# Performance work log

Hardware: AMD Instinct MI355X
Metric: run time of the kernel (lower is better)

## Reference

```python
import jax, jax.numpy as jnp
import numpy as np

B, S, D_MODEL, D_K = 16, 2048, 64, 16
HEAD = D_MODEL * D_K  # 1024, width of each of q, k, v


def setup_inputs() -> dict:
    key = jax.random.key(0)
    kx, kw = jax.random.split(key)
    x = jax.random.normal(kx, (B, S, D_MODEL), dtype=jnp.float32)
    # flax Dense kernel: (in_features, features), no bias
    W = jax.random.normal(kw, (D_MODEL, 3 * HEAD), dtype=jnp.float32) / np.sqrt(D_MODEL)
    return {"x": x, "W": W}


def reference(x, W):
    # fused QKV projection (Dense, no bias)
    qkv = jnp.einsum("bsd,df->bsf", x, W)  # [B, S, 3*HEAD]
    q, k, v = jnp.split(qkv, 3, axis=-1)   # each [B, S, HEAD]

    # q @ k^T over the feature dim -> [B, S, S]
    attn = jnp.einsum("bqd,bkd->bqk", q, k)
    # NOTE: original code scales by sqrt(k.shape[0]) == batch size (kept faithfully)
    d_k = k.shape[0]
    attn = attn / jnp.sqrt(jnp.float32(d_k))
    # original masking: keep upper triangle, then send exact zeros to -9e15
    attn = jnp.triu(attn, k=0)
    attn = jnp.where(attn == 0, jnp.float32(-9000000000000000.0), attn)
    attn = jax.nn.softmax(attn, axis=-1)
    return jnp.einsum("bqk,bkd->bqd", attn, v)  # [B, S, HEAD]
```

## Files before the change

kernel.cpp:

```cpp
#include <hip/hip_runtime.h>
#include <math.h>

#define B_ 16
#define S_ 2048
#define DM_ 64
#define HD_ 1024

typedef float floatx4 __attribute__((ext_vector_type(4)));
typedef short bf16x8 __attribute__((ext_vector_type(8)));
typedef unsigned short ushort4v __attribute__((ext_vector_type(4)));
typedef unsigned short ushort8v __attribute__((ext_vector_type(8)));


__device__ __forceinline__ unsigned short bf_hi(float f) {
    return (unsigned short)((__float_as_uint(f) + 0x8000u) >> 16);
}
__device__ __forceinline__ float bf_f(unsigned short h) {
    return __uint_as_float((unsigned)h << 16);
}
__device__ __forceinline__ void cvt4(floatx4 v, ushort4v& h, ushort4v& l) {
    h[0] = bf_hi(v.x); l[0] = bf_hi(v.x - bf_f(h[0]));
    h[1] = bf_hi(v.y); l[1] = bf_hi(v.y - bf_f(h[1]));
    h[2] = bf_hi(v.z); l[2] = bf_hi(v.z - bf_f(h[2]));
    h[3] = bf_hi(v.w); l[3] = bf_hi(v.w - bf_f(h[3]));
}

#define MFMA(a, b, c) __builtin_amdgcn_mfma_f32_16x16x32_bf16((a), (b), (c), 0, 0, 0)

__device__ __forceinline__ int fragidx(int k, int col) {
    return (((col >> 4) * 2 + (k >> 5)) * 64 + ((k >> 3) & 3) * 16 + (col & 15)) * 8
           + (k & 7);
}

__global__ void k_prep(const float* __restrict__ W, unsigned short* __restrict__ ws) {
    unsigned short* Mfh = ws;
    unsigned short* Mfl = ws + 4096;
    unsigned short* Wfh = ws + 8192;
    unsigned short* Wfl = ws + 73728;
    const int bid = blockIdx.x, t = threadIdx.x;
    if (bid < 64) {
        const int d = bid;
        const int e = t;
        const floatx4* wq = (const floatx4*)(W + (size_t)d * 3072);
        const floatx4* wk = (const floatx4*)(W + (size_t)e * 3072 + 1024);
        floatx4 a = {0.f, 0.f, 0.f, 0.f};
#pragma unroll 4
        for (int j = 0; j < 256; ++j) {
            floatx4 qv = wq[j], kv = wk[j];
            a.x = fmaf(qv.x, kv.x, a.x);
            a.y = fmaf(qv.y, kv.y, a.y);
            a.z = fmaf(qv.z, kv.z, a.z);
            a.w = fmaf(qv.w, kv.w, a.w);
        }
        const float v = (a.x + a.y) + (a.z + a.w);
        const int idx = fragidx(d, e);
        const unsigned short hv = bf_hi(v);
        Mfh[idx] = hv;
        Mfl[idx] = bf_hi(v - bf_f(hv));
    } else {
        const int col = (bid - 64) * 64 + t;
#pragma unroll 8
        for (int k = 0; k < 64; ++k) {
            const float v = W[(size_t)k * 3072 + 2048 + col];
            const int idx = fragidx(k, col);
            const unsigned short hv = bf_hi(v);
            Wfh[idx] = hv;
            Wfl[idx] = bf_hi(v - bf_f(hv));
        }
    }
}

__device__ __forceinline__ void stage_tile(
        unsigned short* xrh, unsigned short* xrl,
        unsigned short* xth, unsigned short* xtl,
        int kg, int dc, floatx4 v0, floatx4 v1, floatx4 v2, floatx4 v3) {
    ushort4v h0, l0, h1, l1, h2, l2, h3, l3;
    cvt4(v0, h0, l0); cvt4(v1, h1, l1);
    cvt4(v2, h2, l2); cvt4(v3, h3, l3);
    *(ushort4v*)(xrh + (4 * kg + 0) * 72 + 4 * dc) = h0;
    *(ushort4v*)(xrh + (4 * kg + 1) * 72 + 4 * dc) = h1;
    *(ushort4v*)(xrh + (4 * kg + 2) * 72 + 4 * dc) = h2;
    *(ushort4v*)(xrh + (4 * kg + 3) * 72 + 4 * dc) = h3;
    *(ushort4v*)(xrl + (4 * kg + 0) * 72 + 4 * dc) = l0;
    *(ushort4v*)(xrl + (4 * kg + 1) * 72 + 4 * dc) = l1;
    *(ushort4v*)(xrl + (4 * kg + 2) * 72 + 4 * dc) = l2;
    *(ushort4v*)(xrl + (4 * kg + 3) * 72 + 4 * dc) = l3;
#pragma unroll
    for (int e = 0; e < 4; ++e) {
        ushort4v th = {h0[e], h1[e], h2[e], h3[e]};
        ushort4v tl = {l0[e], l1[e], l2[e], l3[e]};
        const int rT  = 4 * dc + e;
        const int off = rT * 72 + (((kg >> 1) ^ ((rT >> 3) & 3)) << 3)
                      + ((kg & 1) << 2);
        *(ushort4v*)(xth + off) = th;
        *(ushort4v*)(xtl + off) = tl;
    }
}

__global__ __launch_bounds__(512, 1) void k_fused(
        const float* __restrict__ xg, const unsigned short* __restrict__ wsf,
        float* __restrict__ out) {
    __shared__ __align__(16) unsigned short sm[55296];

    const int tid  = threadIdx.x;
    const int h    = tid >> 8;
    const int lt   = tid & 255;
    const int w    = lt >> 6;
    const int wid  = tid >> 6;
    const int lane = tid & 63;
    const int lm   = lane & 15;
    const int lg   = lane >> 4;

    const int bid = blockIdx.x;
    const int qt  = bid >> 4;
    const int bb  = bid & 15;
    const int q0  = qt * 64;
    const int T   = 32 - qt;
    const int nA  = (T + 1) >> 1;
    const int nOwn = h ? (T - nA) : nA;
    const int kt0  = q0 + (h ? nA * 64 : 0);

    unsigned short* base = sm + h * 23040;
    unsigned short* xrh = base;
    unsigned short* xrl = base + 4608;
    unsigned short* xth = base + 9216;
    unsigned short* xtl = base + 13824;
    unsigned short* Pw  = base + 18432 + w * 1152;
    unsigned short* yh  = sm + 46080;
    unsigned short* yl  = sm + 50688;

    const unsigned short* Mfh = wsf;
    const unsigned short* Mfl = wsf + 4096;
    const unsigned short* Wfh = wsf + 8192;
    const unsigned short* Wfl = wsf + 73728;

    const float* xb = xg + (size_t)bb * S_ * 64;
    const int kg = lt >> 4, dc = lt & 15;

    floatx4 v0, v1, v2, v3;
    if (0 < nOwn) {
        const float* sp = xb + (size_t)(kt0 + kg * 4) * 64 + dc * 4;
        v0 = *(const floatx4*)(sp);
        v1 = *(const floatx4*)(sp + 64);
        v2 = *(const floatx4*)(sp + 128);
        v3 = *(const floatx4*)(sp + 192);
        stage_tile(xrh, xrl, xth, xtl, kg, dc, v0, v1, v2, v3);
    }
    if (1 < nOwn) {
        const float* sp = xb + (size_t)(kt0 + 64 + kg * 4) * 64 + dc * 4;
        v0 = *(const floatx4*)(sp);
        v1 = *(const floatx4*)(sp + 64);
        v2 = *(const floatx4*)(sp + 128);
        v3 = *(const floatx4*)(sp + 192);
    }
    __syncthreads();

    {
        const int rt = wid & 3;
        const int cp = wid >> 2;
        bf16x8 axh[2], axl[2];
#pragma unroll
        for (int kc = 0; kc < 2; ++kc) {
            const int off = (16 * rt + lm) * 72 + 32 * kc + 8 * lg;
            axh[kc] = *(const bf16x8*)(sm + off);
            axl[kc] = *(const bf16x8*)(sm + 4608 + off);
        }
#pragma unroll
        for (int cc = 0; cc < 2; ++cc) {
            const int ct = cp * 2 + cc;
            floatx4 yC = {0.f, 0.f, 0.f, 0.f};
#pragma unroll
            for (int kc = 0; kc < 2; ++kc) {
                bf16x8 bh = *(const bf16x8*)(Mfh + ((ct * 2 + kc) * 64 + lane) * 8);
                bf16x8 bl = *(const bf16x8*)(Mfl + ((ct * 2 + kc) * 64 + lane) * 8);
                yC = MFMA(axh[kc], bh, yC);
                yC = MFMA(axh[kc], bl, yC);
                yC = MFMA(axl[kc], bh, yC);
            }
#pragma unroll
            for (int r = 0; r < 4; ++r) {
                const float vv = yC[r];
                const unsigned short hv = bf_hi(vv);
                const int o = (16 * rt + 4 * lg + r) * 72 + ct * 16 + lm;
                yh[o] = hv;
                yl[o] = bf_hi(vv - bf_f(hv));
            }
        }
    }
    __syncthreads();

    bf16x8 aqh[2], aql[2];
#pragma unroll
    for (int kc = 0; kc < 2; ++kc) {
        const int off = (16 * w + lm) * 72 + 32 * kc + 8 * lg;
        aqh[kc] = *(const bf16x8*)(yh + off);
        aql[kc] = *(const bf16x8*)(yl + off);
    }

    floatx4 U[4];
    float m[4], lsum[4];
#pragma unroll
    for (int r = 0; r < 4; ++r) { m[r] = -INFINITY; lsum[r] = 0.f; }
#pragma unroll
    for (int c = 0; c < 4; ++c) U[c] = (floatx4){0.f, 0.f, 0.f, 0.f};

    for (int t = 0; t < nA; ++t) {
        const int kt = kt0 + t * 64;
        if (t < nOwn) {
            floatx4 Sc[4] = {{0.f,0.f,0.f,0.f},{0.f,0.f,0.f,0.f},
                             {0.f,0.f,0.f,0.f},{0.f,0.f,0.f,0.f}};
#pragma unroll
            for (int kc = 0; kc < 2; ++kc) {
#pragma unroll
                for (int c = 0; c < 4; ++c) {
                    const int ro = (lm + 16 * c) * 72 + 32 * kc + 8 * lg;
                    bf16x8 bh = *(const bf16x8*)(xrh + ro);
                    bf16x8 bl = *(const bf16x8*)(xrl + ro);
                    Sc[c] = MFMA(aqh[kc], bh, Sc[c]);
                    Sc[c] = MFMA(aqh[kc], bl, Sc[c]);
                    Sc[c] = MFMA(aql[kc], bh, Sc[c]);
                }
            }

            float p[4][4], alpha[4];
#pragma unroll
            for (int r = 0; r < 4; ++r) {
                const int ig = q0 + 16 * w + 4 * lg + r;
                float sv[4];
                float rmax = -INFINITY;
#pragma unroll
                for (int c = 0; c < 4; ++c) {
                    const int jg = kt + lm + 16 * c;
                    float v = Sc[c][r] * 0.25f;
                    if (jg < ig || v == 0.0f) v = -9.0e15f;
                    sv[c] = v;
                    rmax = fmaxf(rmax, v);
                }
                rmax = fmaxf(rmax, __shfl_xor(rmax, 1));
                rmax = fmaxf(rmax, __shfl_xor(rmax, 2));
                rmax = fmaxf(rmax, __shfl_xor(rmax, 4));
                rmax = fmaxf(rmax, __shfl_xor(rmax, 8));
                const float mnew = fmaxf(m[r], rmax);
                alpha[r] = __expf(m[r] - mnew);
                float ps = 0.f;
#pragma unroll
                for (int c = 0; c < 4; ++c) {
                    const float pv = __expf(sv[c] - mnew);
                    p[r][c] = pv;
                    ps += pv;
                }
                m[r] = mnew;
                lsum[r] = lsum[r] * alpha[r] + ps;
            }

#pragma unroll
            for (int r = 0; r < 4; ++r)
#pragma unroll
                for (int c = 0; c < 4; ++c)
                    Pw[(4 * lg + r) * 72 + lm + 16 * c] = bf_hi(p[r][c]);

            floatx4 av = {alpha[0], alpha[1], alpha[2], alpha[3]};
#pragma unroll
            for (int c = 0; c < 4; ++c) U[c] *= av;

#pragma unroll
            for (int kc = 0; kc < 2; ++kc) {
                bf16x8 ap = *(const bf16x8*)(Pw + lm * 72 + 32 * kc + 8 * lg);
#pragma unroll
                for (int c = 0; c < 4; ++c) {
                    const int d   = lm + 16 * c;
                    const int blk = (4 * kc + lg) ^ ((d >> 3) & 3);
                    const int off = d * 72 + blk * 8;
                    bf16x8 bh = *(const bf16x8*)(xth + off);
                    bf16x8 bl = *(const bf16x8*)(xtl + off);
                    U[c] = MFMA(ap, bh, U[c]);
                    U[c] = MFMA(ap, bl, U[c]);
                }
            }
        }

        if (t + 1 < nA) {
            __syncthreads();
            if (t + 1 < nOwn)
                stage_tile(xrh, xrl, xth, xtl, kg, dc, v0, v1, v2, v3);
            if (t + 2 < nOwn) {
                const float* sp = xb + (size_t)(kt + 128 + kg * 4) * 64 + dc * 4;
                v0 = *(const floatx4*)(sp);
                v1 = *(const floatx4*)(sp + 64);
                v2 = *(const floatx4*)(sp + 128);
                v3 = *(const floatx4*)(sp + 192);
            }
            __syncthreads();
        }
    }

    float lf[4];
#pragma unroll
    for (int r = 0; r < 4; ++r) {
        float s2 = lsum[r];
        s2 += __shfl_xor(s2, 1);
        s2 += __shfl_xor(s2, 2);
        s2 += __shfl_xor(s2, 4);
        s2 += __shfl_xor(s2, 8);
        lf[r] = s2;
    }

    __syncthreads();
    float* sc = (float*)sm;
    unsigned short* Unh = sm + 23040;
    unsigned short* Unl = sm + 27648;
    if (h == 1) {
        float* bp = sc + lt * 24;
        *(floatx4*)(bp)     = (floatx4){m[0], m[1], m[2], m[3]};
        *(floatx4*)(bp + 4) = (floatx4){lf[0], lf[1], lf[2], lf[3]};
#pragma unroll
        for (int c = 0; c < 4; ++c) *(floatx4*)(bp + 8 + 4 * c) = U[c];
    }
    __syncthreads();
    if (h == 0) {
        const float* bp = sc + lt * 24;
        floatx4 mB = *(const floatx4*)(bp);
        floatx4 lB = *(const floatx4*)(bp + 4);
        floatx4 UB[4];
#pragma unroll
        for (int c = 0; c < 4; ++c) UB[c] = *(const floatx4*)(bp + 8 + 4 * c);
        float eA[4], eB[4], inv[4];
#pragma unroll
        for (int r = 0; r < 4; ++r) {
            const float mT = fmaxf(m[r], mB[r]);
            eA[r] = __expf(m[r] - mT);
            eB[r] = __expf(mB[r] - mT);
            const float lT = lf[r] * eA[r] + lB[r] * eB[r];
            inv[r] = 1.0f / lT;
        }
#pragma unroll
        for (int r = 0; r < 4; ++r)
#pragma unroll
            for (int c = 0; c < 4; ++c) {
                const float o = (U[c][r] * eA[r] + UB[c][r] * eB[r]) * inv[r];
                const unsigned short hv = bf_hi(o);
                const int oo = (16 * w + 4 * lg + r) * 72 + lm + 16 * c;
                Unh[oo] = hv;
                Unl[oo] = bf_hi(o - bf_f(hv));
            }
    }
    __syncthreads();

    bf16x8 Ah[4][2], Al[4][2];
#pragma unroll
    for (int rt = 0; rt < 4; ++rt)
#pragma unroll
        for (int kc = 0; kc < 2; ++kc) {
            const int off = (16 * rt + lm) * 72 + 32 * kc + 8 * lg;
            Ah[rt][kc] = *(const bf16x8*)(Unh + off);
            Al[rt][kc] = *(const bf16x8*)(Unl + off);
        }
    const size_t orow0 = (size_t)bb * S_ + q0;
#pragma unroll
    for (int ctl = 0; ctl < 8; ++ctl) {
        const int ct = wid * 8 + ctl;
        bf16x8 Bh0 = *(const bf16x8*)(Wfh + ((ct * 2 + 0) * 64 + lane) * 8);
        bf16x8 Bl0 = *(const bf16x8*)(Wfl + ((ct * 2 + 0) * 64 + lane) * 8);
        bf16x8 Bh1 = *(const bf16x8*)(Wfh + ((ct * 2 + 1) * 64 + lane) * 8);
        bf16x8 Bl1 = *(const bf16x8*)(Wfl + ((ct * 2 + 1) * 64 + lane) * 8);
#pragma unroll
        for (int rt = 0; rt < 4; ++rt) {
            floatx4 C = {0.f, 0.f, 0.f, 0.f};
            C = MFMA(Ah[rt][0], Bh0, C);
            C = MFMA(Ah[rt][0], Bl0, C);
            C = MFMA(Al[rt][0], Bh0, C);
            C = MFMA(Ah[rt][1], Bh1, C);
            C = MFMA(Ah[rt][1], Bl1, C);
            C = MFMA(Al[rt][1], Bh1, C);
#pragma unroll
            for (int r = 0; r < 4; ++r)
                out[(orow0 + 16 * rt + 4 * lg + r) * HD_ + ct * 16 + lm] = C[r];
        }
    }
}

extern "C" void kernel_launch(void* const* d_in, const int* in_sizes, int n_in,
                              void* d_out, int out_size, void* d_ws, size_t ws_size,
                              hipStream_t stream) {
    const float* x = (const float*)d_in[0];
    const float* W = (const float*)d_in[1];
    unsigned short* wsf = (unsigned short*)d_ws;

    k_prep <<<dim3(80),  64,  0, stream>>>(W, wsf);
    k_fused<<<dim3(512), 512, 0, stream>>>(x, wsf, (float*)d_out);
}
```

Before: 232.4 us.

## Precompute bf16 split and transposed x in prep kernel; read K/V tiles from global

The prep kernel now also converts x into bf16 hi/lo halves, in both row-major and transposed layouts, and writes them to the workspace. The fused attention kernel then loads its MFMA B operands straight from global memory instead of staging tiles through LDS. This removes the per-tile conversion, the LDS staging and the block-wide barriers, and shrinks shared memory so more blocks can share a CU. The causal mask comparison is also restricted to the diagonal tile. In exchange, each wave fetches K/V fragments independently through the cache hierarchy, and an extra large workspace write and read pass is added.

```diff
diff --git a/kernel.cpp b/kernel.cpp
--- a/kernel.cpp
+++ b/kernel.cpp
@@ -32,15 +32,21 @@
            + (k & 7);
 }
 
-__global__ void k_prep(const float* __restrict__ W, unsigned short* __restrict__ ws) {
+__global__ __launch_bounds__(256) void k_prep(
+        const float* __restrict__ x, const float* __restrict__ W,
+        unsigned short* __restrict__ ws) {
     unsigned short* Mfh = ws;
     unsigned short* Mfl = ws + 4096;
     unsigned short* Wfh = ws + 8192;
     unsigned short* Wfl = ws + 73728;
+    unsigned short* xh  = ws + 139264;
+    unsigned short* xl  = xh + 2097152;
+    unsigned short* xTh = xl + 2097152;
+    unsigned short* xTl = xTh + 2097152;
     const int bid = blockIdx.x, t = threadIdx.x;
-    if (bid < 64) {
-        const int d = bid;
-        const int e = t;
+    if (bid < 16) {
+        const int d = bid * 4 + (t >> 6);
+        const int e = t & 63;
         const floatx4* wq = (const floatx4*)(W + (size_t)d * 3072);
         const floatx4* wk = (const floatx4*)(W + (size_t)e * 3072 + 1024);
         floatx4 a = {0.f, 0.f, 0.f, 0.f};
@@ -57,8 +63,8 @@
         const unsigned short hv = bf_hi(v);
         Mfh[idx] = hv;
         Mfl[idx] = bf_hi(v - bf_f(hv));
-    } else {
-        const int col = (bid - 64) * 64 + t;
+    } else if (bid < 20) {
+        const int col = (bid - 16) * 256 + t;
 #pragma unroll 8
         for (int k = 0; k < 64; ++k) {
             const float v = W[(size_t)k * 3072 + 2048 + col];
@@ -67,40 +73,42 @@
             Wfh[idx] = hv;
             Wfl[idx] = bf_hi(v - bf_f(hv));
         }
-    }
-}
-
-__device__ __forceinline__ void stage_tile(
-        unsigned short* xrh, unsigned short* xrl,
-        unsigned short* xth, unsigned short* xtl,
-        int kg, int dc, floatx4 v0, floatx4 v1, floatx4 v2, floatx4 v3) {
-    ushort4v h0, l0, h1, l1, h2, l2, h3, l3;
-    cvt4(v0, h0, l0); cvt4(v1, h1, l1);
-    cvt4(v2, h2, l2); cvt4(v3, h3, l3);
-    *(ushort4v*)(xrh + (4 * kg + 0) * 72 + 4 * dc) = h0;
-    *(ushort4v*)(xrh + (4 * kg + 1) * 72 + 4 * dc) = h1;
-    *(ushort4v*)(xrh + (4 * kg + 2) * 72 + 4 * dc) = h2;
-    *(ushort4v*)(xrh + (4 * kg + 3) * 72 + 4 * dc) = h3;
-    *(ushort4v*)(xrl + (4 * kg + 0) * 72 + 4 * dc) = l0;
-    *(ushort4v*)(xrl + (4 * kg + 1) * 72 + 4 * dc) = l1;
-    *(ushort4v*)(xrl + (4 * kg + 2) * 72 + 4 * dc) = l2;
-    *(ushort4v*)(xrl + (4 * kg + 3) * 72 + 4 * dc) = l3;
-#pragma unroll
-    for (int e = 0; e < 4; ++e) {
-        ushort4v th = {h0[e], h1[e], h2[e], h3[e]};
-        ushort4v tl = {l0[e], l1[e], l2[e], l3[e]};
-        const int rT  = 4 * dc + e;
-        const int off = rT * 72 + (((kg >> 1) ^ ((rT >> 3) & 3)) << 3)
-                      + ((kg & 1) << 2);
-        *(ushort4v*)(xth + off) = th;
-        *(ushort4v*)(xtl + off) = tl;
-    }
-}
-
-__global__ __launch_bounds__(512, 1) void k_fused(
-        const float* __restrict__ xg, const unsigned short* __restrict__ wsf,
-        float* __restrict__ out) {
-    __shared__ __align__(16) unsigned short sm[55296];
+    } else {
+        const int xbid = bid - 20;
+        const int bb = xbid >> 5, rb = xbid & 31;
+        const int kg = t >> 4, dc = t & 15;
+        const size_t r0 = (size_t)bb * S_ + rb * 64;
+        const float* sp = x + (r0 + kg * 4) * 64 + dc * 4;
+        floatx4 v0 = *(const floatx4*)(sp);
+        floatx4 v1 = *(const floatx4*)(sp + 64);
+        floatx4 v2 = *(const floatx4*)(sp + 128);
+        floatx4 v3 = *(const floatx4*)(sp + 192);
+        ushort4v h0, l0, h1, l1, h2, l2, h3, l3;
+        cvt4(v0, h0, l0); cvt4(v1, h1, l1);
+        cvt4(v2, h2, l2); cvt4(v3, h3, l3);
+        const size_t ro = (r0 + kg * 4) * 64 + dc * 4;
+        *(ushort4v*)(xh + ro)       = h0;
+        *(ushort4v*)(xh + ro + 64)  = h1;
+        *(ushort4v*)(xh + ro + 128) = h2;
+        *(ushort4v*)(xh + ro + 192) = h3;
+        *(ushort4v*)(xl + ro)       = l0;
+        *(ushort4v*)(xl + ro + 64)  = l1;
+        *(ushort4v*)(xl + ro + 128) = l2;
+        *(ushort4v*)(xl + ro + 192) = l3;
+#pragma unroll
+        for (int e = 0; e < 4; ++e) {
+            ushort4v th = {h0[e], h1[e], h2[e], h3[e]};
+            ushort4v tl = {l0[e], l1[e], l2[e], l3[e]};
+            const size_t to = ((size_t)bb * 64 + dc * 4 + e) * 2048 + rb * 64 + kg * 4;
+            *(ushort4v*)(xTh + to) = th;
+            *(ushort4v*)(xTl + to) = tl;
+        }
+    }
+}
+
+__global__ __launch_bounds__(512, 4) void k_fused(
+        const unsigned short* __restrict__ wsf, float* __restrict__ out) {
+    __shared__ __align__(16) unsigned short sm[21504];
 
     const int tid  = threadIdx.x;
     const int h    = tid >> 8;
@@ -120,40 +128,18 @@
     const int nOwn = h ? (T - nA) : nA;
     const int kt0  = q0 + (h ? nA * 64 : 0);
 
-    unsigned short* base = sm + h * 23040;
-    unsigned short* xrh = base;
-    unsigned short* xrl = base + 4608;
-    unsigned short* xth = base + 9216;
-    unsigned short* xtl = base + 13824;
-    unsigned short* Pw  = base + 18432 + w * 1152;
-    unsigned short* yh  = sm + 46080;
-    unsigned short* yl  = sm + 50688;
+    unsigned short* yh = sm;
+    unsigned short* yl = sm + 4608;
+    unsigned short* Pw = sm + 9216 + wid * 1152;
 
     const unsigned short* Mfh = wsf;
     const unsigned short* Mfl = wsf + 4096;
     const unsigned short* Wfh = wsf + 8192;
     const unsigned short* Wfl = wsf + 73728;
-
-    const float* xb = xg + (size_t)bb * S_ * 64;
-    const int kg = lt >> 4, dc = lt & 15;
-
-    floatx4 v0, v1, v2, v3;
-    if (0 < nOwn) {
-        const float* sp = xb + (size_t)(kt0 + kg * 4) * 64 + dc * 4;
-        v0 = *(const floatx4*)(sp);
-        v1 = *(const floatx4*)(sp + 64);
-        v2 = *(const floatx4*)(sp + 128);
-        v3 = *(const floatx4*)(sp + 192);
-        stage_tile(xrh, xrl, xth, xtl, kg, dc, v0, v1, v2, v3);
-    }
-    if (1 < nOwn) {
-        const float* sp = xb + (size_t)(kt0 + 64 + kg * 4) * 64 + dc * 4;
-        v0 = *(const floatx4*)(sp);
-        v1 = *(const floatx4*)(sp + 64);
-        v2 = *(const floatx4*)(sp + 128);
-        v3 = *(const floatx4*)(sp + 192);
-    }
-    __syncthreads();
+    const unsigned short* xh  = wsf + 139264;
+    const unsigned short* xl  = xh + 2097152;
+    const unsigned short* xTh = xl + 2097152;
+    const unsigned short* xTl = xTh + 2097152;
 
     {
         const int rt = wid & 3;
@@ -161,9 +147,10 @@
         bf16x8 axh[2], axl[2];
 #pragma unroll
         for (int kc = 0; kc < 2; ++kc) {
-            const int off = (16 * rt + lm) * 72 + 32 * kc + 8 * lg;
-            axh[kc] = *(const bf16x8*)(sm + off);
-            axl[kc] = *(const bf16x8*)(sm + 4608 + off);
+            const size_t off =
+                ((size_t)bb * S_ + q0 + 16 * rt + lm) * 64 + 32 * kc + 8 * lg;
+            axh[kc] = *(const bf16x8*)(xh + off);
+            axl[kc] = *(const bf16x8*)(xl + off);
         }
 #pragma unroll
         for (int cc = 0; cc < 2; ++cc) {
@@ -197,6 +184,11 @@
         aql[kc] = *(const bf16x8*)(yl + off);
     }
 
+    const unsigned short* xqh = xh + ((size_t)bb * S_ + lm) * 64 + lg * 8;
+    const unsigned short* xql = xl + ((size_t)bb * S_ + lm) * 64 + lg * 8;
+    const unsigned short* xth = xTh + ((size_t)bb * 64 + lm) * 2048 + lg * 8;
+    const unsigned short* xtl = xTl + ((size_t)bb * 64 + lm) * 2048 + lg * 8;
+
     floatx4 U[4];
     float m[4], lsum[4];
 #pragma unroll
@@ -204,93 +196,78 @@
 #pragma unroll
     for (int c = 0; c < 4; ++c) U[c] = (floatx4){0.f, 0.f, 0.f, 0.f};
 
-    for (int t = 0; t < nA; ++t) {
+    for (int t = 0; t < nOwn; ++t) {
         const int kt = kt0 + t * 64;
-        if (t < nOwn) {
-            floatx4 Sc[4] = {{0.f,0.f,0.f,0.f},{0.f,0.f,0.f,0.f},
-                             {0.f,0.f,0.f,0.f},{0.f,0.f,0.f,0.f}};
-#pragma unroll
-            for (int kc = 0; kc < 2; ++kc) {
-#pragma unroll
-                for (int c = 0; c < 4; ++c) {
-                    const int ro = (lm + 16 * c) * 72 + 32 * kc + 8 * lg;
-                    bf16x8 bh = *(const bf16x8*)(xrh + ro);
-                    bf16x8 bl = *(const bf16x8*)(xrl + ro);
-                    Sc[c] = MFMA(aqh[kc], bh, Sc[c]);
-                    Sc[c] = MFMA(aqh[kc], bl, Sc[c]);
-                    Sc[c] = MFMA(aql[kc], bh, Sc[c]);
-                }
-            }
-
-            float p[4][4], alpha[4];
-#pragma unroll
-            for (int r = 0; r < 4; ++r) {
-                const int ig = q0 + 16 * w + 4 * lg + r;
-                float sv[4];
-                float rmax = -INFINITY;
-#pragma unroll
-                for (int c = 0; c < 4; ++c) {
-                    const int jg = kt + lm + 16 * c;
-                    float v = Sc[c][r] * 0.25f;
-                    if (jg < ig || v == 0.0f) v = -9.0e15f;
-                    sv[c] = v;
-                    rmax = fmaxf(rmax, v);
-                }
-                rmax = fmaxf(rmax, __shfl_xor(rmax, 1));
-                rmax = fmaxf(rmax, __shfl_xor(rmax, 2));
-                rmax = fmaxf(rmax, __shfl_xor(rmax, 4));
-                rmax = fmaxf(rmax, __shfl_xor(rmax, 8));
-                const float mnew = fmaxf(m[r], rmax);
-                alpha[r] = __expf(m[r] - mnew);
-                float ps = 0.f;
-#pragma unroll
-                for (int c = 0; c < 4; ++c) {
-                    const float pv = __expf(sv[c] - mnew);
-                    p[r][c] = pv;
-                    ps += pv;
-                }
-                m[r] = mnew;
-                lsum[r] = lsum[r] * alpha[r] + ps;
-            }
-
-#pragma unroll
-            for (int r = 0; r < 4; ++r)
-#pragma unroll
-                for (int c = 0; c < 4; ++c)
-                    Pw[(4 * lg + r) * 72 + lm + 16 * c] = bf_hi(p[r][c]);
-
-            floatx4 av = {alpha[0], alpha[1], alpha[2], alpha[3]};
-#pragma unroll
-            for (int c = 0; c < 4; ++c) U[c] *= av;
-
-#pragma unroll
-            for (int kc = 0; kc < 2; ++kc) {
-                bf16x8 ap = *(const bf16x8*)(Pw + lm * 72 + 32 * kc + 8 * lg);
-#pragma unroll
-                for (int c = 0; c < 4; ++c) {
-                    const int d   = lm + 16 * c;
-                    const int blk = (4 * kc + lg) ^ ((d >> 3) & 3);
-                    const int off = d * 72 + blk * 8;
-                    bf16x8 bh = *(const bf16x8*)(xth + off);
-                    bf16x8 bl = *(const bf16x8*)(xtl + off);
-                    U[c] = MFMA(ap, bh, U[c]);
-                    U[c] = MFMA(ap, bl, U[c]);
-                }
-            }
-        }
-
-        if (t + 1 < nA) {
-            __syncthreads();
-            if (t + 1 < nOwn)
-                stage_tile(xrh, xrl, xth, xtl, kg, dc, v0, v1, v2, v3);
-            if (t + 2 < nOwn) {
-                const float* sp = xb + (size_t)(kt + 128 + kg * 4) * 64 + dc * 4;
-                v0 = *(const floatx4*)(sp);
-                v1 = *(const floatx4*)(sp + 64);
-                v2 = *(const floatx4*)(sp + 128);
-                v3 = *(const floatx4*)(sp + 192);
-            }
-            __syncthreads();
+
+        floatx4 Sc[4] = {{0.f,0.f,0.f,0.f},{0.f,0.f,0.f,0.f},
+                         {0.f,0.f,0.f,0.f},{0.f,0.f,0.f,0.f}};
+#pragma unroll
+        for (int kc = 0; kc < 2; ++kc) {
+#pragma unroll
+            for (int c = 0; c < 4; ++c) {
+                const size_t o = (size_t)kt * 64 + c * 1024 + kc * 32;
+                bf16x8 bh = *(const bf16x8*)(xqh + o);
+                bf16x8 bl = *(const bf16x8*)(xql + o);
+                Sc[c] = MFMA(aqh[kc], bh, Sc[c]);
+                Sc[c] = MFMA(aqh[kc], bl, Sc[c]);
+                Sc[c] = MFMA(aql[kc], bh, Sc[c]);
+            }
+        }
+
+        const bool diag = (kt == q0);
+        float p[4][4], alpha[4];
+#pragma unroll
+        for (int r = 0; r < 4; ++r) {
+            const int ig = q0 + 16 * w + 4 * lg + r;
+            float sv[4];
+            float rmax = -INFINITY;
+#pragma unroll
+            for (int c = 0; c < 4; ++c) {
+                float v = Sc[c][r] * 0.25f;
+                bool dead = (v == 0.0f);
+                if (diag) dead = dead || ((kt + lm + 16 * c) < ig);
+                if (dead) v = -9.0e15f;
+                sv[c] = v;
+                rmax = fmaxf(rmax, v);
+            }
+            rmax = fmaxf(rmax, __shfl_xor(rmax, 1));
+            rmax = fmaxf(rmax, __shfl_xor(rmax, 2));
+            rmax = fmaxf(rmax, __shfl_xor(rmax, 4));
+            rmax = fmaxf(rmax, __shfl_xor(rmax, 8));
+            const float mnew = fmaxf(m[r], rmax);
+            alpha[r] = __expf(m[r] - mnew);
+            float ps = 0.f;
+#pragma unroll
+            for (int c = 0; c < 4; ++c) {
+                const float pv = __expf(sv[c] - mnew);
+                p[r][c] = pv;
+                ps += pv;
+            }
+            m[r] = mnew;
+            lsum[r] = lsum[r] * alpha[r] + ps;
+        }
+
+#pragma unroll
+        for (int r = 0; r < 4; ++r)
+#pragma unroll
+            for (int c = 0; c < 4; ++c)
+                Pw[(4 * lg + r) * 72 + lm + 16 * c] = bf_hi(p[r][c]);
+
+        floatx4 av = {alpha[0], alpha[1], alpha[2], alpha[3]};
+#pragma unroll
+        for (int c = 0; c < 4; ++c) U[c] *= av;
+
+#pragma unroll
+        for (int kc = 0; kc < 2; ++kc) {
+            bf16x8 ap = *(const bf16x8*)(Pw + lm * 72 + 32 * kc + 8 * lg);
+#pragma unroll
+            for (int c = 0; c < 4; ++c) {
+                const size_t o = (size_t)c * 32768 + kt + kc * 32;
+                bf16x8 bh = *(const bf16x8*)(xth + o);
+                bf16x8 bl = *(const bf16x8*)(xtl + o);
+                U[c] = MFMA(ap, bh, U[c]);
+                U[c] = MFMA(ap, bl, U[c]);
+            }
         }
     }
 
@@ -307,8 +284,8 @@
 
     __syncthreads();
     float* sc = (float*)sm;
-    unsigned short* Unh = sm + 23040;
-    unsigned short* Unl = sm + 27648;
+    unsigned short* Unh = sm + 12288;
+    unsigned short* Unl = sm + 16896;
     if (h == 1) {
         float* bp = sc + lt * 24;
         *(floatx4*)(bp)     = (floatx4){m[0], m[1], m[2], m[3]};
@@ -386,6 +363,6 @@
     const float* W = (const float*)d_in[1];
     unsigned short* wsf = (unsigned short*)d_ws;
 
-    k_prep <<<dim3(80),  64,  0, stream>>>(W, wsf);
-    k_fused<<<dim3(512), 512, 0, stream>>>(x, wsf, (float*)d_out);
-}
+    k_prep <<<dim3(532), 256, 0, stream>>>(x, W, wsf);
+    k_fused<<<dim3(512), 512, 0, stream>>>(wsf, (float*)d_out);
+}
```

After: 345.3 us. 1.49x slower.
